# Optimization experiments

Measured on AMD Instinct MI355X. Metric: run time of the kernel, lower is better.

## Reference

```python
import jax, jax.numpy as jnp
import numpy as np

DELTA = 1e-7
INDEX = (0, 1)  # hops to process, matches init index=[0,1]


def _divide_no_nan(num, den):
    # tf.math.divide_no_nan semantics: 0 where denominator is 0
    safe = jnp.where(den == 0, 1.0, den)
    return jnp.where(den == 0, 0.0, num / safe)


def setup_inputs() -> dict:
    key = jax.random.key(0)
    k1, k2, k3, k4 = jax.random.split(key, 4)
    B, N, F1 = 8, 2048, 4          # F1 = 1 population + 3 SIR features
    T, C = 2, 64                   # hops available, output channels
    input_feature = jax.random.uniform(k1, (B, N, F1), dtype=jnp.float32)
    OD_all = jax.random.uniform(k2, (B, T, N, N), dtype=jnp.float32)
    kernel = jax.random.normal(k3, (3 * 2 ** len(INDEX), C), dtype=jnp.float32)
    bias = jax.random.normal(k4, (C,), dtype=jnp.float32)
    return {"input_feature": input_feature, "OD_all": OD_all,
            "kernel": kernel, "bias": bias}


def reference(input_feature, OD_all, kernel, bias):
    populations = input_feature[:, :, :1]   # [B,N,1]
    SIR = input_feature[:, :, 1:]           # [B,N,F]
    for idx in INDEX:
        OD = OD_all[:, idx]                                  # [B,N,N]
        SIR_n = _divide_no_nan(SIR, DELTA + populations)     # [B,N,F]
        row_sum = jnp.sum(OD, axis=2, keepdims=True)         # [B,N,1]
        ratio = _divide_no_nan(populations, DELTA + row_sum)  # [B,N,1]
        OD = jnp.where(ratio < 1, OD * ratio, OD)            # clip outflow
        OD_out = jnp.sum(OD, axis=2, keepdims=True)          # [B,N,1]
        OD_in = jnp.sum(OD, axis=1)                          # [B,N]
        SIR_in = jnp.einsum('bij,bif->bjf', OD, SIR_n)       # OD^T @ SIR_n
        SIR_stay = SIR - OD_out * SIR_n
        populations = populations - OD_out + OD_in[..., None]
        SIR = jnp.concatenate([SIR_stay, SIR_in], axis=-1)   # doubles F
    output = jnp.einsum('bnf,fc->bnc', SIR, kernel) + bias
    output = jax.nn.relu(output)
    return jnp.concatenate([populations, output], axis=-1)   # [B,N,1+C]
```

## Files before the change

### kernel.cpp

```cpp
#include <hip/hip_runtime.h>


#define DELTA 1e-7f
constexpr int B = 8, N = 2048;
constexpr int NB = B * N;
constexpr int RPB = 64;
constexpr int NRB = N / RPB;

constexpr int ST0_OFF  = 0;
constexpr int PRE_OFF  = ST0_OFF + NB * 4;
constexpr int ST1_OFF  = PRE_OFF + NB * 8;
constexpr int P0_OFF   = ST1_OFF + NB * 8;
constexpr int P1_OFF   = P0_OFF + B * NRB * N * 4;
constexpr int ACC1_OFF = P1_OFF + B * NRB * N * 8;

__device__ __forceinline__ void fma4(float4& a, float s, const float4& w) {
  a.x = fmaf(s, w.x, a.x);
  a.y = fmaf(s, w.y, a.y);
  a.z = fmaf(s, w.z, a.z);
  a.w = fmaf(s, w.w, a.w);
}

__global__ void __launch_bounds__(512) fused0_kernel(const float* __restrict__ OD,
                                                     const float* __restrict__ feat,
                                                     float* __restrict__ part0,
                                                     float* __restrict__ st0) {
  const int tid = threadIdx.x, w = tid >> 6, l = tid & 63;
  const int b = blockIdx.x >> 5, rb = blockIdx.x & 31, i0 = rb * RPB;
  __shared__ float4 ldsfeat[RPB];
  __shared__ float wpart[64];
  __shared__ float4 wv[8];
  if (tid < RPB) ldsfeat[tid] = ((const float4*)feat)[b * N + i0 + tid];
  __syncthreads();

  const float* odbase = OD + ((size_t)(b * 2) * N + i0) * N + w * 256 + l * 4;
  float4 acc[4] = {};
  float4 cur[8], nxt[8];
#pragma unroll
  for (int m = 0; m < 8; ++m) cur[m] = *(const float4*)(odbase + (size_t)m * N);

  for (int g = 0; g < 8; ++g) {
    if (g < 7) {
#pragma unroll
      for (int m = 0; m < 8; ++m)
        nxt[m] = *(const float4*)(odbase + (size_t)((g + 1) * 8 + m) * N);
    }
#pragma unroll
    for (int m = 0; m < 8; ++m) {
      float s = (cur[m].x + cur[m].y) + (cur[m].z + cur[m].w);
#pragma unroll
      for (int off = 32; off; off >>= 1) s += __shfl_down(s, off, 64);
      if (l == 0) wpart[w * 8 + m] = s;
    }
    __syncthreads();
    if (tid < 8) {
      const int r = g * 8 + tid;
      float rs = 0.f;
#pragma unroll
      for (int ww = 0; ww < 8; ++ww) rs += wpart[ww * 8 + tid];
      const float4 f = ldsfeat[r];
      const float pop = f.x;
      const float ratio = pop / (DELTA + rs);
      const float scale = ratio < 1.f ? ratio : 1.f;
      const float inv = 1.f / (DELTA + pop);
      const float odout = scale * rs;
      const float k1 = 1.f - odout * inv;
      ((float4*)st0)[b * N + i0 + r] =
          make_float4(pop - odout, f.y * k1, f.z * k1, f.w * k1);
      wv[tid] = make_float4(scale, scale * f.y * inv, scale * f.z * inv,
                            scale * f.w * inv);
    }
    __syncthreads();
#pragma unroll
    for (int m = 0; m < 8; ++m) {
      const float4 wvm = wv[m];
      fma4(acc[0], cur[m].x, wvm);
      fma4(acc[1], cur[m].y, wvm);
      fma4(acc[2], cur[m].z, wvm);
      fma4(acc[3], cur[m].w, wvm);
    }
    if (g < 7) {
#pragma unroll
      for (int m = 0; m < 8; ++m) cur[m] = nxt[m];
    }
  }
  float4* pb = (float4*)part0 + (size_t)blockIdx.x * N + (w * 256 + l * 4);
#pragma unroll
  for (int c = 0; c < 4; ++c) pb[c] = acc[c];
}

__global__ void __launch_bounds__(256) prep1_kernel(const float* __restrict__ st0,
                                                    const float* __restrict__ part0,
                                                    float* __restrict__ pre1) {
  const int g = blockIdx.x * 256 + threadIdx.x;
  const int b = g >> 11, i = g & (N - 1);
  float4 in = {0.f, 0.f, 0.f, 0.f};
  const float4* p = (const float4*)part0 + (size_t)b * NRB * N + i;
#pragma unroll 8
  for (int rb = 0; rb < NRB; ++rb) {
    const float4 v = p[(size_t)rb * N];
    in.x += v.x; in.y += v.y; in.z += v.z; in.w += v.w;
  }
  const float4 s0 = ((const float4*)st0)[g];
  const float pop = s0.x + in.x;
  const float inv = 1.f / (DELTA + pop);
  float4* o = (float4*)pre1 + (size_t)g * 2;
  o[0] = make_float4(pop, inv, s0.y, s0.z);
  o[1] = make_float4(s0.w, in.y, in.z, in.w);
}

__global__ void __launch_bounds__(512) fused1_kernel(const float* __restrict__ OD,
                                                     const float* __restrict__ pre1,
                                                     float* __restrict__ part1,
                                                     float* __restrict__ st1) {
  const int tid = threadIdx.x, w = tid >> 6, l = tid & 63;
  const int b = blockIdx.x >> 5, rb = blockIdx.x & 31, i0 = rb * RPB;
  __shared__ float ldspre[RPB * 8];
  __shared__ float wpart[64];
  __shared__ float4 wva[8], wvb[8];
  if (tid < 128)
    ((float4*)ldspre)[tid] =
        ((const float4*)(pre1 + (size_t)(b * N + i0) * 8))[tid];
  __syncthreads();

  const float* odbase = OD + ((size_t)(b * 2 + 1) * N + i0) * N + w * 256 + l * 4;
  float4 accA[4] = {}, accB[4] = {};
  float4 cur[8], nxt[8];
#pragma unroll
  for (int m = 0; m < 8; ++m) cur[m] = *(const float4*)(odbase + (size_t)m * N);

  for (int g = 0; g < 8; ++g) {
    if (g < 7) {
#pragma unroll
      for (int m = 0; m < 8; ++m)
        nxt[m] = *(const float4*)(odbase + (size_t)((g + 1) * 8 + m) * N);
    }
#pragma unroll
    for (int m = 0; m < 8; ++m) {
      float s = (cur[m].x + cur[m].y) + (cur[m].z + cur[m].w);
#pragma unroll
      for (int off = 32; off; off >>= 1) s += __shfl_down(s, off, 64);
      if (l == 0) wpart[w * 8 + m] = s;
    }
    __syncthreads();
    if (tid < 8) {
      const int r = g * 8 + tid;
      float rs = 0.f;
#pragma unroll
      for (int ww = 0; ww < 8; ++ww) rs += wpart[ww * 8 + tid];
      const float* pr = &ldspre[r * 8];
      const float pop = pr[0], inv = pr[1];
      const float ratio = pop / (DELTA + rs);
      const float scale = ratio < 1.f ? ratio : 1.f;
      const float odout = scale * rs;
      const float k1 = 1.f - odout * inv;
      float4* s4 = (float4*)st1 + (size_t)(b * N + i0 + r) * 2;
      s4[0] = make_float4(pop - odout, pr[2] * k1, pr[3] * k1, pr[4] * k1);
      s4[1] = make_float4(pr[5] * k1, pr[6] * k1, pr[7] * k1, 0.f);
      const float si = scale * inv;
      wva[tid] = make_float4(scale, pr[2] * si, pr[3] * si, pr[4] * si);
      wvb[tid] = make_float4(pr[5] * si, pr[6] * si, pr[7] * si, 0.f);
    }
    __syncthreads();
#pragma unroll
    for (int m = 0; m < 8; ++m) {
      const float4 wa = wva[m], wb = wvb[m];
      fma4(accA[0], cur[m].x, wa);
      fma4(accB[0], cur[m].x, wb);
      fma4(accA[1], cur[m].y, wa);
      fma4(accB[1], cur[m].y, wb);
      fma4(accA[2], cur[m].z, wa);
      fma4(accB[2], cur[m].z, wb);
      fma4(accA[3], cur[m].w, wa);
      fma4(accB[3], cur[m].w, wb);
    }
    if (g < 7) {
#pragma unroll
      for (int m = 0; m < 8; ++m) cur[m] = nxt[m];
    }
  }
  float4* pb =
      (float4*)part1 + ((size_t)blockIdx.x * N + (w * 256 + l * 4)) * 2;
#pragma unroll
  for (int c = 0; c < 4; ++c) {
    pb[c * 2] = accA[c];
    pb[c * 2 + 1] = accB[c];
  }
}

__global__ void __launch_bounds__(256) reduce1_kernel(const float* __restrict__ part1,
                                                      float* __restrict__ acc1) {
  const int g = blockIdx.x * 256 + threadIdx.x;
  const int b = g >> 11, j = g & (N - 1);
  float4 a = {0.f, 0.f, 0.f, 0.f}, c = {0.f, 0.f, 0.f, 0.f};
  const float4* p = (const float4*)part1 + ((size_t)b * NRB * N + j) * 2;
#pragma unroll 8
  for (int rb = 0; rb < NRB; ++rb) {
    const float4 va = p[(size_t)rb * N * 2];
    const float4 vb = p[(size_t)rb * N * 2 + 1];
    a.x += va.x; a.y += va.y; a.z += va.z; a.w += va.w;
    c.x += vb.x; c.y += vb.y; c.z += vb.z; c.w += vb.w;
  }
  float4* o = (float4*)acc1 + (size_t)g * 2;
  o[0] = a;
  o[1] = c;
}

__global__ void __launch_bounds__(256) final_kernel(const float* __restrict__ st1,
                                                    const float* __restrict__ acc1,
                                                    const float* __restrict__ kern,
                                                    const float* __restrict__ bias,
                                                    float* __restrict__ out) {
  __shared__ float klds[12 * 64];
  const int tid = threadIdx.x;
  if (tid < 192) ((float4*)klds)[tid] = ((const float4*)kern)[tid];
  __syncthreads();
  const int p = blockIdx.x * 4 + (tid >> 6);
  const int c = tid & 63;
  const float4* s4 = (const float4*)st1 + (size_t)p * 2;
  const float4 l0 = s4[0], l1 = s4[1];
  const float4* a4 = (const float4*)acc1 + (size_t)p * 2;
  const float4 a0 = a4[0], a1 = a4[1];
  const float S[12] = {l0.y, l0.z, l0.w, l1.x, l1.y, l1.z,
                       a0.y, a0.z, a0.w, a1.x, a1.y, a1.z};
  float sum = bias[c];
#pragma unroll
  for (int f = 0; f < 12; ++f) sum += S[f] * klds[f * 64 + c];
  float* o = out + (size_t)p * 65;
  o[1 + c] = sum > 0.f ? sum : 0.f;
  if (c == 0) o[0] = l0.x + a0.x;
}

extern "C" void kernel_launch(void* const* d_in, const int* in_sizes, int n_in,
                              void* d_out, int out_size, void* d_ws, size_t ws_size,
                              hipStream_t stream) {
  const float* feat = (const float*)d_in[0];
  const float* OD   = (const float*)d_in[1];
  const float* kern = (const float*)d_in[2];
  const float* bias = (const float*)d_in[3];
  float* out = (float*)d_out;
  float* ws = (float*)d_ws;

  float* st0   = ws + ST0_OFF;
  float* pre1  = ws + PRE_OFF;
  float* st1   = ws + ST1_OFF;
  float* part0 = ws + P0_OFF;
  float* part1 = ws + P1_OFF;
  float* acc1  = ws + ACC1_OFF;

  fused0_kernel<<<B * NRB, 512, 0, stream>>>(OD, feat, part0, st0);
  prep1_kernel<<<NB / 256, 256, 0, stream>>>(st0, part0, pre1);
  fused1_kernel<<<B * NRB, 512, 0, stream>>>(OD, pre1, part1, st1);
  reduce1_kernel<<<NB / 256, 256, 0, stream>>>(part1, acc1);
  final_kernel<<<NB / 4, 256, 0, stream>>>(st1, acc1, kern, bias, out);
}
```

Baseline: 401.7 us.

## Fold partial-sum reductions into fused1 and final kernels, drop prep1/reduce1

Removes the separate prep1 and reduce1 kernels. fused1 now reduces part0 partials for its own 64 rows through shared memory before the main loop. The final kernel reduces the 32 part1 partials with wavefront shuffles before the channel projection. This cuts two launches and the pre1/acc1 intermediate round trips, at the cost of extra redundant-free but serialized prologue work in fused1 and a shuffle reduction in the final kernel.

```diff
diff --git a/kernel.cpp b/kernel.cpp
--- a/kernel.cpp
+++ b/kernel.cpp
@@ -7,18 +7,19 @@
 constexpr int RPB = 64;
 constexpr int NRB = N / RPB;
 
-constexpr int ST0_OFF  = 0;
-constexpr int PRE_OFF  = ST0_OFF + NB * 4;
-constexpr int ST1_OFF  = PRE_OFF + NB * 8;
-constexpr int P0_OFF   = ST1_OFF + NB * 8;
-constexpr int P1_OFF   = P0_OFF + B * NRB * N * 4;
-constexpr int ACC1_OFF = P1_OFF + B * NRB * N * 8;
+constexpr int ST0_OFF = 0;
+constexpr int ST1_OFF = ST0_OFF + NB * 4;
+constexpr int P0_OFF  = ST1_OFF + NB * 8;
+constexpr int P1_OFF  = P0_OFF + B * NRB * N * 4;
 
 __device__ __forceinline__ void fma4(float4& a, float s, const float4& w) {
   a.x = fmaf(s, w.x, a.x);
   a.y = fmaf(s, w.y, a.y);
   a.z = fmaf(s, w.z, a.z);
   a.w = fmaf(s, w.w, a.w);
+}
+__device__ __forceinline__ void add4(float4& a, const float4& v) {
+  a.x += v.x; a.y += v.y; a.z += v.z; a.w += v.w;
 }
 
 __global__ void __launch_bounds__(512) fused0_kernel(const float* __restrict__ OD,
@@ -89,38 +90,39 @@
   for (int c = 0; c < 4; ++c) pb[c] = acc[c];
 }
 
-__global__ void __launch_bounds__(256) prep1_kernel(const float* __restrict__ st0,
-                                                    const float* __restrict__ part0,
-                                                    float* __restrict__ pre1) {
-  const int g = blockIdx.x * 256 + threadIdx.x;
-  const int b = g >> 11, i = g & (N - 1);
-  float4 in = {0.f, 0.f, 0.f, 0.f};
-  const float4* p = (const float4*)part0 + (size_t)b * NRB * N + i;
-#pragma unroll 8
-  for (int rb = 0; rb < NRB; ++rb) {
-    const float4 v = p[(size_t)rb * N];
-    in.x += v.x; in.y += v.y; in.z += v.z; in.w += v.w;
-  }
-  const float4 s0 = ((const float4*)st0)[g];
-  const float pop = s0.x + in.x;
-  const float inv = 1.f / (DELTA + pop);
-  float4* o = (float4*)pre1 + (size_t)g * 2;
-  o[0] = make_float4(pop, inv, s0.y, s0.z);
-  o[1] = make_float4(s0.w, in.y, in.z, in.w);
-}
-
 __global__ void __launch_bounds__(512) fused1_kernel(const float* __restrict__ OD,
-                                                     const float* __restrict__ pre1,
+                                                     const float* __restrict__ st0,
+                                                     const float* __restrict__ part0,
                                                      float* __restrict__ part1,
                                                      float* __restrict__ st1) {
   const int tid = threadIdx.x, w = tid >> 6, l = tid & 63;
   const int b = blockIdx.x >> 5, rb = blockIdx.x & 31, i0 = rb * RPB;
   __shared__ float ldspre[RPB * 8];
+  __shared__ float4 redp[8][RPB];
   __shared__ float wpart[64];
   __shared__ float4 wva[8], wvb[8];
-  if (tid < 128)
-    ((float4*)ldspre)[tid] =
-        ((const float4*)(pre1 + (size_t)(b * N + i0) * 8))[tid];
+
+  {
+    const int row = tid & 63, rbg = tid >> 6;
+    const float4* p0 = (const float4*)part0 + (size_t)b * NRB * N + i0 + row;
+    float4 s = {0.f, 0.f, 0.f, 0.f};
+#pragma unroll
+    for (int k = 0; k < 4; ++k) add4(s, p0[(size_t)(rbg * 4 + k) * N]);
+    redp[rbg][row] = s;
+  }
+  __syncthreads();
+  if (tid < RPB) {
+    float4 in = redp[0][tid];
+#pragma unroll
+    for (int g = 1; g < 8; ++g) add4(in, redp[g][tid]);
+    const float4 s0 = ((const float4*)st0)[b * N + i0 + tid];
+    const float pop = s0.x + in.x;
+    const float inv = 1.f / (DELTA + pop);
+    float* o = &ldspre[tid * 8];
+    o[0] = pop; o[1] = inv;
+    o[2] = s0.y; o[3] = s0.z; o[4] = s0.w;
+    o[5] = in.y; o[6] = in.z; o[7] = in.w;
+  }
   __syncthreads();
 
   const float* odbase = OD + ((size_t)(b * 2 + 1) * N + i0) * N + w * 256 + l * 4;
@@ -179,8 +181,7 @@
       for (int m = 0; m < 8; ++m) cur[m] = nxt[m];
     }
   }
-  float4* pb =
-      (float4*)part1 + ((size_t)blockIdx.x * N + (w * 256 + l * 4)) * 2;
+  float4* pb = (float4*)part1 + ((size_t)blockIdx.x * N + (w * 256 + l * 4)) * 2;
 #pragma unroll
   for (int c = 0; c < 4; ++c) {
     pb[c * 2] = accA[c];
@@ -188,47 +189,47 @@
   }
 }
 
-__global__ void __launch_bounds__(256) reduce1_kernel(const float* __restrict__ part1,
-                                                      float* __restrict__ acc1) {
-  const int g = blockIdx.x * 256 + threadIdx.x;
-  const int b = g >> 11, j = g & (N - 1);
-  float4 a = {0.f, 0.f, 0.f, 0.f}, c = {0.f, 0.f, 0.f, 0.f};
-  const float4* p = (const float4*)part1 + ((size_t)b * NRB * N + j) * 2;
-#pragma unroll 8
-  for (int rb = 0; rb < NRB; ++rb) {
-    const float4 va = p[(size_t)rb * N * 2];
-    const float4 vb = p[(size_t)rb * N * 2 + 1];
-    a.x += va.x; a.y += va.y; a.z += va.z; a.w += va.w;
-    c.x += vb.x; c.y += vb.y; c.z += vb.z; c.w += vb.w;
-  }
-  float4* o = (float4*)acc1 + (size_t)g * 2;
-  o[0] = a;
-  o[1] = c;
-}
-
-__global__ void __launch_bounds__(256) final_kernel(const float* __restrict__ st1,
-                                                    const float* __restrict__ acc1,
-                                                    const float* __restrict__ kern,
-                                                    const float* __restrict__ bias,
-                                                    float* __restrict__ out) {
+__global__ void __launch_bounds__(256) final2_kernel(const float* __restrict__ st1,
+                                                     const float* __restrict__ part1,
+                                                     const float* __restrict__ kern,
+                                                     const float* __restrict__ bias,
+                                                     float* __restrict__ out) {
   __shared__ float klds[12 * 64];
-  const int tid = threadIdx.x;
+  __shared__ float s12[4][16];
+  const int tid = threadIdx.x, quad = tid >> 6, c = tid & 63;
   if (tid < 192) ((float4*)klds)[tid] = ((const float4*)kern)[tid];
-  __syncthreads();
-  const int p = blockIdx.x * 4 + (tid >> 6);
-  const int c = tid & 63;
-  const float4* s4 = (const float4*)st1 + (size_t)p * 2;
-  const float4 l0 = s4[0], l1 = s4[1];
-  const float4* a4 = (const float4*)acc1 + (size_t)p * 2;
-  const float4 a0 = a4[0], a1 = a4[1];
-  const float S[12] = {l0.y, l0.z, l0.w, l1.x, l1.y, l1.z,
-                       a0.y, a0.z, a0.w, a1.x, a1.y, a1.z};
+
+  const int p = blockIdx.x * 4 + quad;
+  const int b = p >> 11, n = p & (N - 1);
+  float4 v = ((const float4*)part1)[(((size_t)(b * NRB + (c >> 1)) * N + n) << 1) + (c & 1)];
+#pragma unroll
+  for (int off = 32; off >= 2; off >>= 1) {
+    v.x += __shfl_down(v.x, off, 64);
+    v.y += __shfl_down(v.y, off, 64);
+    v.z += __shfl_down(v.z, off, 64);
+    v.w += __shfl_down(v.w, off, 64);
+  }
+  if (c == 0) {
+    const float4 s0 = ((const float4*)st1)[(size_t)p * 2];
+    const float4 s1 = ((const float4*)st1)[(size_t)p * 2 + 1];
+    float* o = s12[quad];
+    o[0] = s0.y; o[1] = s0.z; o[2] = s0.w;
+    o[3] = s1.x; o[4] = s1.y; o[5] = s1.z;
+    o[6] = v.y;  o[7] = v.z;  o[8] = v.w;
+    o[12] = s0.x + v.x;
+  }
+  if (c == 1) {
+    float* o = s12[quad];
+    o[9] = v.x; o[10] = v.y; o[11] = v.z;
+  }
+  __syncthreads();
+
   float sum = bias[c];
 #pragma unroll
-  for (int f = 0; f < 12; ++f) sum += S[f] * klds[f * 64 + c];
+  for (int f = 0; f < 12; ++f) sum += s12[quad][f] * klds[f * 64 + c];
   float* o = out + (size_t)p * 65;
   o[1 + c] = sum > 0.f ? sum : 0.f;
-  if (c == 0) o[0] = l0.x + a0.x;
+  if (c == 0) o[0] = s12[quad][12];
 }
 
 extern "C" void kernel_launch(void* const* d_in, const int* in_sizes, int n_in,
@@ -242,15 +243,11 @@
   float* ws = (float*)d_ws;
 
   float* st0   = ws + ST0_OFF;
-  float* pre1  = ws + PRE_OFF;
   float* st1   = ws + ST1_OFF;
   float* part0 = ws + P0_OFF;
   float* part1 = ws + P1_OFF;
-  float* acc1  = ws + ACC1_OFF;
 
   fused0_kernel<<<B * NRB, 512, 0, stream>>>(OD, feat, part0, st0);
-  prep1_kernel<<<NB / 256, 256, 0, stream>>>(st0, part0, pre1);
-  fused1_kernel<<<B * NRB, 512, 0, stream>>>(OD, pre1, part1, st1);
-  reduce1_kernel<<<NB / 256, 256, 0, stream>>>(part1, acc1);
-  final_kernel<<<NB / 4, 256, 0, stream>>>(st1, acc1, kern, bias, out);
-}
+  fused1_kernel<<<B * NRB, 512, 0, stream>>>(OD, st0, part0, part1, st1);
+  final2_kernel<<<NB / 4, 256, 0, stream>>>(st1, part1, kern, bias, out);
+}
```

Result: no change. 398.3 us (-0.8%).
